# Optimization experiments

Hardware: AMD Instinct MI355X
Metric: run time of the kernel (lower is better)

The kernel has to match this reference:

```python
import jax, jax.numpy as jnp
import numpy as np

N_NODES = 4096
N_GRAPHS = 32
N = N_NODES * N_GRAPHS          # 131072 total nodes
DEG = 32
E = N * DEG                      # 4194304 edges
IN_CH = 16
OUT_CH = 2
EPS_BN = 1e-5


def setup_inputs() -> dict:
    key = jax.random.key(0)
    ks = jax.random.split(key, 24)
    rn = lambda k, s, scale=0.1: (jax.random.normal(k, s, dtype=jnp.float32) * scale)
    return {
        "x": jax.random.normal(ks[0], (N, IN_CH), dtype=jnp.float32),
        "edge_index": jax.random.randint(ks[1], (2, E), 0, N),
        "edge_attr": jax.random.uniform(ks[2], (E, 3), dtype=jnp.float32),
        # GraphConv1: 16 -> 20  (lin_rel has bias, lin_root has no bias; PyG GraphConv)
        "W_rel1": rn(ks[3], (IN_CH, 20)), "b1": jnp.zeros((20,), jnp.float32), "W_root1": rn(ks[4], (IN_CH, 20)),
        # GraphConv2: 20 -> 20
        "W_rel2": rn(ks[5], (20, 20)), "b2": jnp.zeros((20,), jnp.float32), "W_root2": rn(ks[6], (20, 20)),
        # GraphConv3: 20 -> 1
        "W_rel3": rn(ks[7], (20, 1)), "b3": jnp.zeros((1,), jnp.float32), "W_root3": rn(ks[8], (20, 1)),
        # BatchNorm1d(num_nodes) affine params (channel dim = node index)
        "bn1_g": jnp.ones((N_NODES,), jnp.float32), "bn1_b": jnp.zeros((N_NODES,), jnp.float32),
        "bn2_g": jnp.ones((N_NODES,), jnp.float32), "bn2_b": jnp.zeros((N_NODES,), jnp.float32),
        # fc layers, stored [in, out]
        "fc1_W": rn(ks[9], (N_NODES, 50), 0.02), "fc1_b": jnp.zeros((50,), jnp.float32),
        "fc2_W": rn(ks[10], (50, OUT_CH)), "fc2_b": jnp.zeros((OUT_CH,), jnp.float32),
        "num_graphs": N_GRAPHS,
    }


def _graph_conv(x, src, dst, w, W_rel, b_rel, W_root):
    # PyG GraphConv: out_i = lin_root(x_i) + lin_rel( sum_{j->i} w_ji * x_j )
    msg = x[src] * w[:, None]                              # [E, F] gather + scale
    agg = jax.ops.segment_sum(msg, dst, num_segments=x.shape[0])  # scatter-add
    return agg @ W_rel + b_rel + x @ W_root


def _bn_nodes(h3, gamma, beta):
    # BatchNorm1d(num_nodes) in training mode: h3 is [B, num_nodes, F];
    # normalize per node-channel over (batch, feat), biased variance (torch training).
    mu = jnp.mean(h3, axis=(0, 2), keepdims=True)
    var = jnp.var(h3, axis=(0, 2), keepdims=True)
    hn = (h3 - mu) * jax.lax.rsqrt(var + EPS_BN)
    return hn * gamma[None, :, None] + beta[None, :, None]


def reference(x, edge_index, edge_attr,
              W_rel1, b1, W_root1, W_rel2, b2, W_root2, W_rel3, b3, W_root3,
              bn1_g, bn1_b, bn2_g, bn2_b, fc1_W, fc1_b, fc2_W, fc2_b, num_graphs):
    src, dst = edge_index[0], edge_index[1]
    w = edge_attr[:, 2]
    B = num_graphs

    h = _graph_conv(x, src, dst, w, W_rel1, b1, W_root1)
    h = jax.nn.leaky_relu(h)                                   # slope 0.01, matches torch default
    h = _bn_nodes(h.reshape(B, -1, h.shape[-1]), bn1_g, bn1_b).reshape(-1, h.shape[-1])

    h = _graph_conv(h, src, dst, w, W_rel2, b2, W_root2)
    h = jax.nn.leaky_relu(h)
    h = _bn_nodes(h.reshape(B, -1, h.shape[-1]), bn2_g, bn2_b).reshape(-1, h.shape[-1])

    h = _graph_conv(h, src, dst, w, W_rel3, b3, W_root3)
    h = jax.nn.leaky_relu(h)
    h = h.reshape(B, -1)                                        # [B, num_nodes]

    # per-graph normalization; note: divides by var (not std), var is unbiased (torch.var default)
    eps = 1e-10
    out = (h - jnp.mean(h, axis=1, keepdims=True)) / (jnp.var(h, axis=1, keepdims=True, ddof=1) + eps)
    out = jax.nn.leaky_relu(out @ fc1_W + fc1_b)
    # dropout omitted (eval-mode identity)
    out = out @ fc2_W + fc2_b
    return (out, h)
```

## Files before the change

kernel.cpp:

```cpp
#include <hip/hip_runtime.h>
#include <hip/hip_fp16.h>

#define N_NODES 4096
#define N_GRAPHS 32
#define NTOT (N_NODES * N_GRAPHS)
#define NE (NTOT * 32)
#define C1 16
#define C2 20
#define CAP 72

#define NBUCK 512
#define BSHIFT 8
#define BMASK 255
#define CAPB 8960
#define EPB1 8192

__device__ __forceinline__ float lrelu(float v) { return v > 0.f ? v : 0.01f * v; }

__device__ __forceinline__ unsigned pack_edge(int src, float w) {
    int k = __float2int_rn(w * 32768.f);
    if (k > 32767) k = 32767;
    return (unsigned)src | ((unsigned)k << 17);
}
__device__ __forceinline__ void unpack_edge(unsigned p, int& src, float& w) {
    src = (int)(p & 0x1FFFFu);
    w = (float)(p >> 17) * 3.0517578125e-5f;
}

__device__ __forceinline__ uint4 pack8h(const float* v) {
    union { uint4 u4; __half h[8]; } c;
#pragma unroll
    for (int q = 0; q < 8; q++) c.h[q] = __float2half(v[q]);
    return c.u4;
}
__device__ __forceinline__ uint2 pack4h(const float* v) {
    union { uint2 u2; __half h[4]; } c;
#pragma unroll
    for (int q = 0; q < 4; q++) c.h[q] = __float2half(v[q]);
    return c.u2;
}
__device__ __forceinline__ void fma8(uint4 u, float wv, float* acc) {
    union { uint4 u4; __half2 h2[4]; } c; c.u4 = u;
#pragma unroll
    for (int q = 0; q < 4; q++) {
        float2 f = __half22float2(c.h2[q]);
        acc[2 * q]     += f.x * wv;
        acc[2 * q + 1] += f.y * wv;
    }
}
__device__ __forceinline__ void fma4(uint2 u, float wv, float* acc) {
    union { uint2 u2; __half2 h2[2]; } c; c.u2 = u;
#pragma unroll
    for (int q = 0; q < 2; q++) {
        float2 f = __half22float2(c.h2[q]);
        acc[2 * q]     += f.x * wv;
        acc[2 * q + 1] += f.y * wv;
    }
}
__device__ __forceinline__ void unp8(uint4 u, float* v) {
    union { uint4 u4; __half2 h2[4]; } c; c.u4 = u;
#pragma unroll
    for (int q = 0; q < 4; q++) {
        float2 f = __half22float2(c.h2[q]);
        v[2 * q] = f.x; v[2 * q + 1] = f.y;
    }
}
__device__ __forceinline__ void unp4(uint2 u, float* v) {
    union { uint2 u2; __half2 h2[2]; } c; c.u2 = u;
#pragma unroll
    for (int q = 0; q < 2; q++) {
        float2 f = __half22float2(c.h2[q]);
        v[2 * q] = f.x; v[2 * q + 1] = f.y;
    }
}

__global__ __launch_bounds__(256) void k_part1(const int* __restrict__ ei,
                                               const float* __restrict__ ea,
                                               int* __restrict__ gcur,
                                               uint2* __restrict__ part) {
    __shared__ unsigned lrecA[EPB1];
    __shared__ unsigned char lrecB[EPB1];
    __shared__ int hist[NBUCK], sscan[NBUCK], base[NBUCK], lcur[NBUCK];
    __shared__ int ts[256];
    int t = threadIdx.x;
    hist[t] = 0; hist[t + 256] = 0;
    __syncthreads();
    int eb = blockIdx.x * EPB1;
    int dreg[EPB1 / 256];
#pragma unroll
    for (int i = 0; i < EPB1 / 256; i++) {
        int d = ei[NE + eb + i * 256 + t];
        dreg[i] = d;
        atomicAdd(&hist[d >> BSHIFT], 1);
    }
    __syncthreads();
    int a0 = hist[2 * t], a1 = hist[2 * t + 1];
    ts[t] = a0 + a1;
    __syncthreads();
    for (int d = 1; d < 256; d <<= 1) {
        int v = (t >= d) ? ts[t - d] : 0;
        __syncthreads();
        ts[t] += v;
        __syncthreads();
    }
    int excl = (t == 0) ? 0 : ts[t - 1];
    sscan[2 * t] = excl;
    sscan[2 * t + 1] = excl + a0;
    lcur[2 * t] = excl;
    lcur[2 * t + 1] = excl + a0;
    base[t]       = atomicAdd(&gcur[t], hist[t]);
    base[t + 256] = atomicAdd(&gcur[t + 256], hist[t + 256]);
    __syncthreads();
#pragma unroll
    for (int i = 0; i < EPB1 / 256; i++) {
        int e = eb + i * 256 + t;
        int d = dreg[i];
        int b = d >> BSHIFT;
        int pos = atomicAdd(&lcur[b], 1);
        lrecA[pos] = pack_edge(ei[e], ea[3 * e + 2]);
        lrecB[pos] = (unsigned char)(d & BMASK);
    }
    __syncthreads();
    for (int j = t; j < EPB1; j += 256) {
        int lo = 0, hi = NBUCK - 1;
        while (lo < hi) { int mid = (lo + hi + 1) >> 1; if (sscan[mid] <= j) lo = mid; else hi = mid - 1; }
        int b = lo;
        int dp = base[b] + (j - sscan[b]);
        if (dp < CAPB) part[(size_t)b * CAPB + dp] = make_uint2(lrecA[j], (unsigned)lrecB[j]);
    }
}

__global__ __launch_bounds__(256) void k_part2(const int* __restrict__ gcur,
                                               const uint2* __restrict__ part,
                                               unsigned* __restrict__ slots,
                                               int* __restrict__ cnt) {
    __shared__ int cur[256];
    int t = threadIdx.x;
    cur[t] = 0;
    __syncthreads();
    int b = blockIdx.x;
    int nrec = gcur[b]; if (nrec > CAPB) nrec = CAPB;
    const uint2* rp = part + (size_t)b * CAPB;
    int nb = b << BSHIFT;
    for (int i = t; i < nrec; i += 256) {
        uint2 r = rp[i];
        int ld = (int)r.y;
        int pos = atomicAdd(&cur[ld], 1);
        if (pos < CAP) slots[(size_t)pos * NTOT + nb + ld] = r.x;
    }
    __syncthreads();
    cnt[nb + t] = cur[t];
}

__global__ void k_fill_slots(const int* __restrict__ ei, const float* __restrict__ ea,
                             int* __restrict__ cnt, unsigned* __restrict__ slots) {
    int e = blockIdx.x * 256 + threadIdx.x;
    if (e >= NE) return;
    int d = ei[NE + e];
    int pos = atomicAdd(&cnt[d], 1);
    if (pos < CAP) slots[(size_t)pos * NTOT + d] = pack_edge(ei[e], ea[3 * e + 2]);
}

__global__ void k_xcast(const float* __restrict__ x, uint4* __restrict__ xa, uint4* __restrict__ xb) {
    int n = blockIdx.x * 256 + threadIdx.x;
    if (n >= NTOT) return;
    float xr[C1];
    const float4* xp = (const float4*)(x + (size_t)n * C1);
#pragma unroll
    for (int q = 0; q < 4; q++) ((float4*)xr)[q] = xp[q];
    xa[n] = pack8h(xr);
    xb[n] = pack8h(xr + 8);
}

__global__ __launch_bounds__(256) void k_conv1(const uint4* __restrict__ xa, const uint4* __restrict__ xb,
                        const unsigned* __restrict__ slots, const int* __restrict__ cnt,
                        const float* __restrict__ Wr, const float* __restrict__ bb,
                        const float* __restrict__ Wo, float* __restrict__ t1) {
    __shared__ float sWr[C1 * C2], sWo[C1 * C2], sb[C2];
    __shared__ float sacc[4][64][8];
    for (int k = threadIdx.x; k < C1 * C2; k += 256) { sWr[k] = Wr[k]; sWo[k] = Wo[k]; }
    if (threadIdx.x < C2) sb[threadIdx.x] = bb[threadIdx.x];
    int nl = threadIdx.x & 63;
    int sub = threadIdx.x >> 6;
    int gn = blockIdx.x * 64 + nl;
    int m = cnt[gn]; if (m > CAP) m = CAP;
    int h0 = m >> 1;
    int lo = (sub & 1) ? h0 : 0;
    int hi = (sub & 1) ? m : h0;
    const uint4* va = (sub < 2) ? xa : xb;
    float acc[8];
#pragma unroll
    for (int q = 0; q < 8; q++) acc[q] = 0.f;
    int i = lo;
    for (; i + 4 <= hi; i += 4) {
        unsigned p0 = __builtin_nontemporal_load(slots + (size_t)(i + 0) * NTOT + gn);
        unsigned p1 = __builtin_nontemporal_load(slots + (size_t)(i + 1) * NTOT + gn);
        unsigned p2 = __builtin_nontemporal_load(slots + (size_t)(i + 2) * NTOT + gn);
        unsigned p3 = __builtin_nontemporal_load(slots + (size_t)(i + 3) * NTOT + gn);
        int s0, s1, s2, s3; float w0, w1, w2, w3;
        unpack_edge(p0, s0, w0); unpack_edge(p1, s1, w1);
        unpack_edge(p2, s2, w2); unpack_edge(p3, s3, w3);
        uint4 u0 = va[s0], u1 = va[s1], u2 = va[s2], u3 = va[s3];
        fma8(u0, w0, acc); fma8(u1, w1, acc); fma8(u2, w2, acc); fma8(u3, w3, acc);
    }
    for (; i < hi; i++) {
        unsigned p = __builtin_nontemporal_load(slots + (size_t)i * NTOT + gn);
        int s; float w; unpack_edge(p, s, w);
        fma8(va[s], w, acc);
    }
#pragma unroll
    for (int q = 0; q < 8; q++) sacc[sub][nl][q] = acc[q];
    __syncthreads();
    int n2 = threadIdx.x >> 2, qq = threadIdx.x & 3;
    int gn2 = blockIdx.x * 64 + n2;
    float accf[C1];
#pragma unroll
    for (int q = 0; q < 8; q++) accf[q] = sacc[0][n2][q] + sacc[1][n2][q];
#pragma unroll
    for (int q = 0; q < 8; q++) accf[8 + q] = sacc[2][n2][q] + sacc[3][n2][q];
    float xr[C1];
    unp8(xa[gn2], xr); unp8(xb[gn2], xr + 8);
    float outv[5];
#pragma unroll
    for (int jj = 0; jj < 5; jj++) {
        int j = qq * 5 + jj;
        float a = sb[j];
#pragma unroll
        for (int q = 0; q < C1; q++) a += accf[q] * sWr[q * C2 + j] + xr[q] * sWo[q * C2 + j];
        outv[jj] = lrelu(a);
    }
#pragma unroll
    for (int jj = 0; jj < 5; jj++) t1[(size_t)gn2 * C2 + qq * 5 + jj] = outv[jj];
}

__global__ void k_stats(const float* __restrict__ t, float* __restrict__ mu, float* __restrict__ rs) {
    int i = blockIdx.x;
    float s = 0.f, ss = 0.f;
    for (int k = threadIdx.x; k < N_GRAPHS * C2; k += 64) {
        int g = k / C2, j = k - g * C2;
        float v = t[((size_t)(g * N_NODES + i)) * C2 + j];
        s += v; ss += v * v;
    }
#pragma unroll
    for (int off = 32; off > 0; off >>= 1) { s += __shfl_down(s, off); ss += __shfl_down(ss, off); }
    if (threadIdx.x == 0) {
        float m = s * (1.f / (N_GRAPHS * C2));
        float var = ss * (1.f / (N_GRAPHS * C2)) - m * m;
        mu[i] = m;
        rs[i] = rsqrtf(var + 1e-5f);
    }
}

__global__ void k_bn_apply(const float* __restrict__ t, const float* __restrict__ mu,
                           const float* __restrict__ rs, const float* __restrict__ gam,
                           const float* __restrict__ bet, uint4* __restrict__ hnA,
                           uint2* __restrict__ hnB) {
    int n = blockIdx.x * 256 + threadIdx.x;
    if (n >= NTOT) return;
    int i = n & (N_NODES - 1);
    float sc = rs[i] * gam[i];
    float sh = bet[i] - mu[i] * sc;
    float v[C2];
    const float4* tp = (const float4*)(t + (size_t)n * C2);
#pragma unroll
    for (int q = 0; q < 5; q++) ((float4*)v)[q] = tp[q];
#pragma unroll
    for (int j = 0; j < C2; j++) v[j] = v[j] * sc + sh;
    hnA[n] = pack8h(v);
    uint2* hp = hnB + (size_t)n * 3;
    hp[0] = pack4h(v + 8);
    hp[1] = pack4h(v + 12);
    hp[2] = pack4h(v + 16);
}

__global__ __launch_bounds__(256) void k_conv2(const uint4* __restrict__ hnA,
                        const uint2* __restrict__ hnB,
                        const unsigned* __restrict__ slots, const int* __restrict__ cnt,
                        const float* __restrict__ Wr, const float* __restrict__ bb,
                        const float* __restrict__ Wo, float* __restrict__ t2) {
    __shared__ float sWr[C2 * C2], sWo[C2 * C2], sb[C2];
    __shared__ float saccA[2][64][8];
    __shared__ float saccB[2][64][12];
    for (int k = threadIdx.x; k < C2 * C2; k += 256) { sWr[k] = Wr[k]; sWo[k] = Wo[k]; }
    if (threadIdx.x < C2) sb[threadIdx.x] = bb[threadIdx.x];
    int nl = threadIdx.x & 63;
    int sub = threadIdx.x >> 6;
    int gn = blockIdx.x * 64 + nl;
    int m = cnt[gn]; if (m > CAP) m = CAP;
    int h0 = m >> 1;
    int lo = (sub & 1) ? h0 : 0;
    int hi = (sub & 1) ? m : h0;
    if (sub < 2) {
        float acc[8];
#pragma unroll
        for (int q = 0; q < 8; q++) acc[q] = 0.f;
        int i = lo;
        for (; i + 4 <= hi; i += 4) {
            unsigned p0 = __builtin_nontemporal_load(slots + (size_t)(i + 0) * NTOT + gn);
            unsigned p1 = __builtin_nontemporal_load(slots + (size_t)(i + 1) * NTOT + gn);
            unsigned p2 = __builtin_nontemporal_load(slots + (size_t)(i + 2) * NTOT + gn);
            unsigned p3 = __builtin_nontemporal_load(slots + (size_t)(i + 3) * NTOT + gn);
            int s0, s1, s2, s3; float w0, w1, w2, w3;
            unpack_edge(p0, s0, w0); unpack_edge(p1, s1, w1);
            unpack_edge(p2, s2, w2); unpack_edge(p3, s3, w3);
            uint4 u0 = hnA[s0], u1 = hnA[s1], u2 = hnA[s2], u3 = hnA[s3];
            fma8(u0, w0, acc); fma8(u1, w1, acc); fma8(u2, w2, acc); fma8(u3, w3, acc);
        }
        for (; i < hi; i++) {
            unsigned p = __builtin_nontemporal_load(slots + (size_t)i * NTOT + gn);
            int s; float w; unpack_edge(p, s, w);
            fma8(hnA[s], w, acc);
        }
#pragma unroll
        for (int q = 0; q < 8; q++) saccA[sub][nl][q] = acc[q];
    } else {
        float acc[12];
#pragma unroll
        for (int q = 0; q < 12; q++) acc[q] = 0.f;
        int i = lo;
        for (; i + 4 <= hi; i += 4) {
            unsigned p0 = __builtin_nontemporal_load(slots + (size_t)(i + 0) * NTOT + gn);
            unsigned p1 = __builtin_nontemporal_load(slots + (size_t)(i + 1) * NTOT + gn);
            unsigned p2 = __builtin_nontemporal_load(slots + (size_t)(i + 2) * NTOT + gn);
            unsigned p3 = __builtin_nontemporal_load(slots + (size_t)(i + 3) * NTOT + gn);
            int s0, s1, s2, s3; float w0, w1, w2, w3;
            unpack_edge(p0, s0, w0); unpack_edge(p1, s1, w1);
            unpack_edge(p2, s2, w2); unpack_edge(p3, s3, w3);
            const uint2* r0 = hnB + (size_t)s0 * 3;
            const uint2* r1 = hnB + (size_t)s1 * 3;
            const uint2* r2 = hnB + (size_t)s2 * 3;
            const uint2* r3 = hnB + (size_t)s3 * 3;
            uint2 a0 = r0[0], b0 = r0[1], c0 = r0[2];
            uint2 a1 = r1[0], b1 = r1[1], c1 = r1[2];
            uint2 a2 = r2[0], b2 = r2[1], c2 = r2[2];
            uint2 a3 = r3[0], b3 = r3[1], c3 = r3[2];
            fma4(a0, w0, acc); fma4(b0, w0, acc + 4); fma4(c0, w0, acc + 8);
            fma4(a1, w1, acc); fma4(b1, w1, acc + 4); fma4(c1, w1, acc + 8);
            fma4(a2, w2, acc); fma4(b2, w2, acc + 4); fma4(c2, w2, acc + 8);
            fma4(a3, w3, acc); fma4(b3, w3, acc + 4); fma4(c3, w3, acc + 8);
        }
        for (; i < hi; i++) {
            unsigned p = __builtin_nontemporal_load(slots + (size_t)i * NTOT + gn);
            int s; float w; unpack_edge(p, s, w);
            const uint2* r = hnB + (size_t)s * 3;
            fma4(r[0], w, acc); fma4(r[1], w, acc + 4); fma4(r[2], w, acc + 8);
        }
#pragma unroll
        for (int q = 0; q < 12; q++) saccB[sub - 2][nl][q] = acc[q];
    }
    __syncthreads();
    int n2 = threadIdx.x >> 2, qq = threadIdx.x & 3;
    int gn2 = blockIdx.x * 64 + n2;
    float accf[C2];
#pragma unroll
    for (int q = 0; q < 8; q++) accf[q] = saccA[0][n2][q] + saccA[1][n2][q];
#pragma unroll
    for (int q = 0; q < 12; q++) accf[8 + q] = saccB[0][n2][q] + saccB[1][n2][q];
    float h[C2];
    unp8(hnA[gn2], h);
    {
        const uint2* r = hnB + (size_t)gn2 * 3;
        unp4(r[0], h + 8); unp4(r[1], h + 12); unp4(r[2], h + 16);
    }
    float outv[5];
#pragma unroll
    for (int jj = 0; jj < 5; jj++) {
        int j = qq * 5 + jj;
        float a = sb[j];
#pragma unroll
        for (int q = 0; q < C2; q++) a += accf[q] * sWr[q * C2 + j] + h[q] * sWo[q * C2 + j];
        outv[jj] = lrelu(a);
    }
#pragma unroll
    for (int jj = 0; jj < 5; jj++) t2[(size_t)gn2 * C2 + qq * 5 + jj] = outv[jj];
}

__global__ void k_bn2_proj(const float* __restrict__ t, const float* __restrict__ mu,
                           const float* __restrict__ rs, const float* __restrict__ gam,
                           const float* __restrict__ bet, const float* __restrict__ Wr3,
                           const float* __restrict__ b3, const float* __restrict__ Wo3,
                           float* __restrict__ y, float* __restrict__ r2) {
    __shared__ float sWr[C2], sWo[C2];
    if (threadIdx.x < C2) { sWr[threadIdx.x] = Wr3[threadIdx.x]; sWo[threadIdx.x] = Wo3[threadIdx.x]; }
    __syncthreads();
    int n = blockIdx.x * 256 + threadIdx.x;
    if (n >= NTOT) return;
    int i = n & (N_NODES - 1);
    float sc = rs[i] * gam[i];
    float sh = bet[i] - mu[i] * sc;
    float v[C2];
    const float4* tp = (const float4*)(t + (size_t)n * C2);
#pragma unroll
    for (int q = 0; q < 5; q++) ((float4*)v)[q] = tp[q];
    float ay = 0.f, ar = 0.f;
#pragma unroll
    for (int j = 0; j < C2; j++) {
        float hv = v[j] * sc + sh;
        ay += hv * sWr[j];
        ar += hv * sWo[j];
    }
    y[n] = ay;
    r2[n] = ar + b3[0];
}

__global__ __launch_bounds__(256) void k_conv3(const float* __restrict__ y, const float* __restrict__ r2,
                        const unsigned* __restrict__ slots, const int* __restrict__ cnt,
                        float* __restrict__ hout, float* __restrict__ gsum, float* __restrict__ gss) {
    __shared__ float pbuf[2][128];
    __shared__ float ls[4], lss[4];
    int nl = threadIdx.x & 127;
    int half = threadIdx.x >> 7;
    int n = blockIdx.x * 128 + nl;
    int m = cnt[n]; if (m > CAP) m = CAP;
    int h0 = m >> 1;
    int lo = half ? h0 : 0;
    int hi = half ? m : h0;
    float a = 0.f;
    int i = lo;
    for (; i + 4 <= hi; i += 4) {
        unsigned p0 = __builtin_nontemporal_load(slots + (size_t)(i + 0) * NTOT + n);
        unsigned p1 = __builtin_nontemporal_load(slots + (size_t)(i + 1) * NTOT + n);
        unsigned p2 = __builtin_nontemporal_load(slots + (size_t)(i + 2) * NTOT + n);
        unsigned p3 = __builtin_nontemporal_load(slots + (size_t)(i + 3) * NTOT + n);
        int s0, s1, s2, s3; float w0, w1, w2, w3;
        unpack_edge(p0, s0, w0); unpack_edge(p1, s1, w1);
        unpack_edge(p2, s2, w2); unpack_edge(p3, s3, w3);
        a += y[s0] * w0 + y[s1] * w1 + y[s2] * w2 + y[s3] * w3;
    }
    for (; i < hi; i++) {
        unsigned p = __builtin_nontemporal_load(slots + (size_t)i * NTOT + n);
        int s; float w; unpack_edge(p, s, w);
        a += y[s] * w;
    }
    pbuf[half][nl] = a;
    __syncthreads();
    float v = 0.f;
    if (half == 0) {
        v = lrelu(pbuf[0][nl] + pbuf[1][nl] + r2[n]);
        hout[n] = v;
    }
    float s = v, ss = v * v;
#pragma unroll
    for (int o = 32; o > 0; o >>= 1) { s += __shfl_down(s, o); ss += __shfl_down(ss, o); }
    int wid = threadIdx.x >> 6, lid = threadIdx.x & 63;
    if (lid == 0) { ls[wid] = s; lss[wid] = ss; }
    __syncthreads();
    if (threadIdx.x == 0) {
        int g = blockIdx.x >> 5;
        atomicAdd(&gsum[g], ls[0] + ls[1] + ls[2] + ls[3]);
        atomicAdd(&gss[g], lss[0] + lss[1] + lss[2] + lss[3]);
    }
}

__global__ void k_fc1(const float* __restrict__ h, const float* __restrict__ gsum,
                      const float* __restrict__ gss, const float* __restrict__ W,
                      const float* __restrict__ b, float* __restrict__ z) {
    __shared__ float ls[4];
    int blk = blockIdx.x;
    int g = blk / 50, k = blk - g * 50;
    float mu = gsum[g] / N_NODES;
    float var = (gss[g] - N_NODES * mu * mu) / (N_NODES - 1);
    float inv = 1.f / (var + 1e-10f);
    const float* hr = h + (size_t)g * N_NODES;
    float p = 0.f;
    for (int n = threadIdx.x; n < N_NODES; n += 256)
        p += (hr[n] - mu) * inv * W[(size_t)n * 50 + k];
#pragma unroll
    for (int off = 32; off > 0; off >>= 1) p += __shfl_down(p, off);
    int wid = threadIdx.x >> 6, lid = threadIdx.x & 63;
    if (lid == 0) ls[wid] = p;
    __syncthreads();
    if (threadIdx.x == 0) {
        float S = ls[0] + ls[1] + ls[2] + ls[3];
        z[g * 50 + k] = lrelu(S + b[k]);
    }
}

__global__ void k_fc2(const float* __restrict__ z, const float* __restrict__ W,
                      const float* __restrict__ b, float* __restrict__ out) {
    int t = threadIdx.x;
    if (t >= N_GRAPHS * 2) return;
    int g = t >> 1, o = t & 1;
    float acc = b[o];
#pragma unroll
    for (int k = 0; k < 50; k++) acc += z[g * 50 + k] * W[k * 2 + o];
    out[g * 2 + o] = acc;
}

extern "C" void kernel_launch(void* const* d_in, const int* in_sizes, int n_in,
                              void* d_out, int out_size, void* d_ws, size_t ws_size,
                              hipStream_t stream) {
    const float* x    = (const float*)d_in[0];
    const int*   ei   = (const int*)d_in[1];
    const float* ea   = (const float*)d_in[2];
    const float* Wr1  = (const float*)d_in[3];
    const float* b1   = (const float*)d_in[4];
    const float* Wo1  = (const float*)d_in[5];
    const float* Wr2  = (const float*)d_in[6];
    const float* b2   = (const float*)d_in[7];
    const float* Wo2  = (const float*)d_in[8];
    const float* Wr3  = (const float*)d_in[9];
    const float* b3   = (const float*)d_in[10];
    const float* Wo3  = (const float*)d_in[11];
    const float* bn1g = (const float*)d_in[12];
    const float* bn1b = (const float*)d_in[13];
    const float* bn2g = (const float*)d_in[14];
    const float* bn2b = (const float*)d_in[15];
    const float* fc1W = (const float*)d_in[16];
    const float* fc1b = (const float*)d_in[17];
    const float* fc2W = (const float*)d_in[18];
    const float* fc2b = (const float*)d_in[19];
    float* out = (float*)d_out;

    const size_t part_bytes  = (size_t)NBUCK * CAPB * sizeof(uint2);
    const size_t slots_bytes = (size_t)NTOT * CAP * sizeof(unsigned);
    const size_t tail_bytes  = (size_t)NTOT * C2 * sizeof(float)
                             + (size_t)NTOT * 16 * 3
                             + (size_t)NTOT * 24
                             + (size_t)NTOT * 2 * sizeof(float)
                             + (size_t)NTOT * sizeof(int)
                             + (size_t)(NBUCK + 4 * N_NODES + 8 * N_GRAPHS + N_GRAPHS * 50 + 64) * sizeof(float);
    const bool useSort = ws_size >= part_bytes + slots_bytes + tail_bytes;

    char* wsb = (char*)d_ws;
    uint2*    part  = (uint2*)wsb;     wsb += useSort ? part_bytes : 0;
    unsigned* slots = (unsigned*)wsb;  wsb += slots_bytes;
    float*    bufA  = (float*)wsb;     wsb += (size_t)NTOT * C2 * sizeof(float);
    uint4*    xa    = (uint4*)wsb;     wsb += (size_t)NTOT * 16;
    uint4*    xb    = (uint4*)wsb;     wsb += (size_t)NTOT * 16;
    uint4*    hnA   = (uint4*)wsb;     wsb += (size_t)NTOT * 16;
    uint2*    hnB   = (uint2*)wsb;     wsb += (size_t)NTOT * 24;
    float*    yv    = (float*)wsb;     wsb += (size_t)NTOT * sizeof(float);
    float*    r2v   = (float*)wsb;     wsb += (size_t)NTOT * sizeof(float);
    int*      cnt   = (int*)wsb;       wsb += (size_t)NTOT * sizeof(int);
    int*      gcur  = (int*)wsb;       wsb += NBUCK * sizeof(int);
    float*    mu1   = (float*)wsb;     wsb += N_NODES * sizeof(float);
    float*    rs1   = (float*)wsb;     wsb += N_NODES * sizeof(float);
    float*    mu2   = (float*)wsb;     wsb += N_NODES * sizeof(float);
    float*    rs2   = (float*)wsb;     wsb += N_NODES * sizeof(float);
    float*    gsum  = (float*)wsb;     wsb += N_GRAPHS * sizeof(float);
    float*    gss   = (float*)wsb;     wsb += N_GRAPHS * sizeof(float);
    float*    z     = (float*)wsb;     wsb += N_GRAPHS * 50 * sizeof(float);

    const int EB = (NE + 255) / 256;
    const int NB = (NTOT + 255) / 256;

    hipMemsetAsync(gsum, 0, 2 * N_GRAPHS * sizeof(float), stream);
    k_xcast<<<NB, 256, 0, stream>>>(x, xa, xb);
    if (useSort) {
        hipMemsetAsync(gcur, 0, NBUCK * sizeof(int), stream);
        k_part1<<<NE / EPB1, 256, 0, stream>>>(ei, ea, gcur, part);
        k_part2<<<NBUCK, 256, 0, stream>>>(gcur, part, slots, cnt);
    } else {
        hipMemsetAsync(cnt, 0, (size_t)NTOT * sizeof(int), stream);
        k_fill_slots<<<EB, 256, 0, stream>>>(ei, ea, cnt, slots);
    }

    k_conv1<<<NTOT / 64, 256, 0, stream>>>(xa, xb, slots, cnt, Wr1, b1, Wo1, bufA);
    k_stats<<<N_NODES, 64, 0, stream>>>(bufA, mu1, rs1);
    k_bn_apply<<<NB, 256, 0, stream>>>(bufA, mu1, rs1, bn1g, bn1b, hnA, hnB);

    k_conv2<<<NTOT / 64, 256, 0, stream>>>(hnA, hnB, slots, cnt, Wr2, b2, Wo2, bufA);
    k_stats<<<N_NODES, 64, 0, stream>>>(bufA, mu2, rs2);
    k_bn2_proj<<<NB, 256, 0, stream>>>(bufA, mu2, rs2, bn2g, bn2b, Wr3, b3, Wo3, yv, r2v);

    k_conv3<<<NTOT / 128, 256, 0, stream>>>(yv, r2v, slots, cnt, out + 64, gsum, gss);

    k_fc1<<<N_GRAPHS * 50, 256, 0, stream>>>(out + 64, gsum, gss, fc1W, fc1b, z);
    k_fc2<<<1, 64, 0, stream>>>(z, fc2W, fc2b, out);
}
```

Measured before the change: 488.9 us.

## Stage slot scatter in LDS and restructure conv gathers with deeper unrolling

k_part2 now splits each bucket across two blocks and builds the per-destination slot tile in shared memory, then writes it out row-coalesced instead of scattering 4-byte stores directly to global. The conv1/conv2 kernels switch to 128 nodes per block with two threads per node, each gathering all feature chunks over half the edges, using 8-way unrolled gather helpers. The conv2 feature layout is changed from three 8-byte pieces per node to one 16-byte plus one 8-byte array, cutting the number of load instructions. The edge-slot loads are now read once per feature chunk, which adds repeated slot traffic, and the shared tile uses about 37 KB of LDS per block, limiting occupancy.

Measured after the change: 512.7 us. +4.9%, slower.

```diff
diff --git a/kernel.cpp b/kernel.cpp
--- a/kernel.cpp
+++ b/kernel.cpp
@@ -71,6 +71,47 @@
     for (int q = 0; q < 2; q++) {
         float2 f = __half22float2(c.h2[q]);
         v[2 * q] = f.x; v[2 * q + 1] = f.y;
+    }
+}
+
+__device__ __forceinline__ void gather16(const uint4* __restrict__ arr,
+                                         const unsigned* __restrict__ slots,
+                                         int gn, int lo, int hi, float* acc) {
+    int i = lo;
+    for (; i + 8 <= hi; i += 8) {
+        unsigned p[8];
+#pragma unroll
+        for (int k = 0; k < 8; k++) p[k] = __builtin_nontemporal_load(slots + (size_t)(i + k) * NTOT + gn);
+        uint4 u[8]; float w[8];
+#pragma unroll
+        for (int k = 0; k < 8; k++) { int s; unpack_edge(p[k], s, w[k]); u[k] = arr[s]; }
+#pragma unroll
+        for (int k = 0; k < 8; k++) fma8(u[k], w[k], acc);
+    }
+    for (; i < hi; i++) {
+        unsigned p = __builtin_nontemporal_load(slots + (size_t)i * NTOT + gn);
+        int s; float w; unpack_edge(p, s, w);
+        fma8(arr[s], w, acc);
+    }
+}
+__device__ __forceinline__ void gather8(const uint2* __restrict__ arr,
+                                        const unsigned* __restrict__ slots,
+                                        int gn, int lo, int hi, float* acc) {
+    int i = lo;
+    for (; i + 8 <= hi; i += 8) {
+        unsigned p[8];
+#pragma unroll
+        for (int k = 0; k < 8; k++) p[k] = __builtin_nontemporal_load(slots + (size_t)(i + k) * NTOT + gn);
+        uint2 u[8]; float w[8];
+#pragma unroll
+        for (int k = 0; k < 8; k++) { int s; unpack_edge(p[k], s, w[k]); u[k] = arr[s]; }
+#pragma unroll
+        for (int k = 0; k < 8; k++) fma4(u[k], w[k], acc);
+    }
+    for (; i < hi; i++) {
+        unsigned p = __builtin_nontemporal_load(slots + (size_t)i * NTOT + gn);
+        int s; float w; unpack_edge(p, s, w);
+        fma4(arr[s], w, acc);
     }
 }
 
@@ -134,22 +175,35 @@
                                                const uint2* __restrict__ part,
                                                unsigned* __restrict__ slots,
                                                int* __restrict__ cnt) {
-    __shared__ int cur[256];
+    __shared__ unsigned tile[128 * CAP];
+    __shared__ int cur[128];
+    __shared__ int maxc;
     int t = threadIdx.x;
-    cur[t] = 0;
-    __syncthreads();
-    int b = blockIdx.x;
+    if (t < 128) cur[t] = 0;
+    if (t == 0) maxc = 0;
+    __syncthreads();
+    int b = blockIdx.x >> 1;
+    int halfsel = blockIdx.x & 1;
+    int nbase = (b << BSHIFT) + (halfsel << 7);
     int nrec = gcur[b]; if (nrec > CAPB) nrec = CAPB;
     const uint2* rp = part + (size_t)b * CAPB;
-    int nb = b << BSHIFT;
     for (int i = t; i < nrec; i += 256) {
         uint2 r = rp[i];
         int ld = (int)r.y;
-        int pos = atomicAdd(&cur[ld], 1);
-        if (pos < CAP) slots[(size_t)pos * NTOT + nb + ld] = r.x;
-    }
-    __syncthreads();
-    cnt[nb + t] = cur[t];
+        if ((ld >> 7) == halfsel) {
+            int l = ld & 127;
+            int pos = atomicAdd(&cur[l], 1);
+            if (pos < CAP) tile[pos * 128 + l] = r.x;
+        }
+    }
+    __syncthreads();
+    if (t < 128) { cnt[nbase + t] = cur[t]; atomicMax(&maxc, cur[t]); }
+    __syncthreads();
+    int mc = maxc; if (mc > CAP) mc = CAP;
+    for (int j = t; j < mc * 128; j += 256) {
+        int pos = j >> 7, l = j & 127;
+        slots[(size_t)pos * NTOT + nbase + l] = tile[j];
+    }
 }
 
 __global__ void k_fill_slots(const int* __restrict__ ei, const float* __restrict__ ea,
@@ -177,60 +231,42 @@
                         const float* __restrict__ Wr, const float* __restrict__ bb,
                         const float* __restrict__ Wo, float* __restrict__ t1) {
     __shared__ float sWr[C1 * C2], sWo[C1 * C2], sb[C2];
-    __shared__ float sacc[4][64][8];
+    __shared__ float sacc[2][128][17];
     for (int k = threadIdx.x; k < C1 * C2; k += 256) { sWr[k] = Wr[k]; sWo[k] = Wo[k]; }
     if (threadIdx.x < C2) sb[threadIdx.x] = bb[threadIdx.x];
-    int nl = threadIdx.x & 63;
-    int sub = threadIdx.x >> 6;
-    int gn = blockIdx.x * 64 + nl;
+    int nl = threadIdx.x & 127;
+    int half = threadIdx.x >> 7;
+    int gn = blockIdx.x * 128 + nl;
     int m = cnt[gn]; if (m > CAP) m = CAP;
     int h0 = m >> 1;
-    int lo = (sub & 1) ? h0 : 0;
-    int hi = (sub & 1) ? m : h0;
-    const uint4* va = (sub < 2) ? xa : xb;
-    float acc[8];
-#pragma unroll
-    for (int q = 0; q < 8; q++) acc[q] = 0.f;
-    int i = lo;
-    for (; i + 4 <= hi; i += 4) {
-        unsigned p0 = __builtin_nontemporal_load(slots + (size_t)(i + 0) * NTOT + gn);
-        unsigned p1 = __builtin_nontemporal_load(slots + (size_t)(i + 1) * NTOT + gn);
-        unsigned p2 = __builtin_nontemporal_load(slots + (size_t)(i + 2) * NTOT + gn);
-        unsigned p3 = __builtin_nontemporal_load(slots + (size_t)(i + 3) * NTOT + gn);
-        int s0, s1, s2, s3; float w0, w1, w2, w3;
-        unpack_edge(p0, s0, w0); unpack_edge(p1, s1, w1);
-        unpack_edge(p2, s2, w2); unpack_edge(p3, s3, w3);
-        uint4 u0 = va[s0], u1 = va[s1], u2 = va[s2], u3 = va[s3];
-        fma8(u0, w0, acc); fma8(u1, w1, acc); fma8(u2, w2, acc); fma8(u3, w3, acc);
-    }
-    for (; i < hi; i++) {
-        unsigned p = __builtin_nontemporal_load(slots + (size_t)i * NTOT + gn);
-        int s; float w; unpack_edge(p, s, w);
-        fma8(va[s], w, acc);
-    }
-#pragma unroll
-    for (int q = 0; q < 8; q++) sacc[sub][nl][q] = acc[q];
-    __syncthreads();
-    int n2 = threadIdx.x >> 2, qq = threadIdx.x & 3;
-    int gn2 = blockIdx.x * 64 + n2;
+    int lo = half ? h0 : 0;
+    int hi = half ? m : h0;
+    float acc[C1];
+#pragma unroll
+    for (int q = 0; q < C1; q++) acc[q] = 0.f;
+    gather16(xa, slots, gn, lo, hi, acc);
+    gather16(xb, slots, gn, lo, hi, acc + 8);
+#pragma unroll
+    for (int q = 0; q < C1; q++) sacc[half][nl][q] = acc[q];
+    __syncthreads();
+    int n2 = threadIdx.x >> 1, oh = threadIdx.x & 1;
+    int gn2 = blockIdx.x * 128 + n2;
     float accf[C1];
 #pragma unroll
-    for (int q = 0; q < 8; q++) accf[q] = sacc[0][n2][q] + sacc[1][n2][q];
-#pragma unroll
-    for (int q = 0; q < 8; q++) accf[8 + q] = sacc[2][n2][q] + sacc[3][n2][q];
+    for (int q = 0; q < C1; q++) accf[q] = sacc[0][n2][q] + sacc[1][n2][q];
     float xr[C1];
     unp8(xa[gn2], xr); unp8(xb[gn2], xr + 8);
-    float outv[5];
-#pragma unroll
-    for (int jj = 0; jj < 5; jj++) {
-        int j = qq * 5 + jj;
+    float outv[10];
+#pragma unroll
+    for (int jj = 0; jj < 10; jj++) {
+        int j = oh * 10 + jj;
         float a = sb[j];
 #pragma unroll
         for (int q = 0; q < C1; q++) a += accf[q] * sWr[q * C2 + j] + xr[q] * sWo[q * C2 + j];
         outv[jj] = lrelu(a);
     }
 #pragma unroll
-    for (int jj = 0; jj < 5; jj++) t1[(size_t)gn2 * C2 + qq * 5 + jj] = outv[jj];
+    for (int jj = 0; jj < 10; jj++) t1[(size_t)gn2 * C2 + oh * 10 + jj] = outv[jj];
 }
 
 __global__ void k_stats(const float* __restrict__ t, float* __restrict__ mu, float* __restrict__ rs) {
@@ -254,7 +290,7 @@
 __global__ void k_bn_apply(const float* __restrict__ t, const float* __restrict__ mu,
                            const float* __restrict__ rs, const float* __restrict__ gam,
                            const float* __restrict__ bet, uint4* __restrict__ hnA,
-                           uint2* __restrict__ hnB) {
+                           uint4* __restrict__ hnB1, uint2* __restrict__ hnB2) {
     int n = blockIdx.x * 256 + threadIdx.x;
     if (n >= NTOT) return;
     int i = n & (N_NODES - 1);
@@ -267,112 +303,53 @@
 #pragma unroll
     for (int j = 0; j < C2; j++) v[j] = v[j] * sc + sh;
     hnA[n] = pack8h(v);
-    uint2* hp = hnB + (size_t)n * 3;
-    hp[0] = pack4h(v + 8);
-    hp[1] = pack4h(v + 12);
-    hp[2] = pack4h(v + 16);
+    hnB1[n] = pack8h(v + 8);
+    hnB2[n] = pack4h(v + 16);
 }
 
 __global__ __launch_bounds__(256) void k_conv2(const uint4* __restrict__ hnA,
-                        const uint2* __restrict__ hnB,
+                        const uint4* __restrict__ hnB1, const uint2* __restrict__ hnB2,
                         const unsigned* __restrict__ slots, const int* __restrict__ cnt,
                         const float* __restrict__ Wr, const float* __restrict__ bb,
                         const float* __restrict__ Wo, float* __restrict__ t2) {
     __shared__ float sWr[C2 * C2], sWo[C2 * C2], sb[C2];
-    __shared__ float saccA[2][64][8];
-    __shared__ float saccB[2][64][12];
+    __shared__ float sacc[2][128][21];
     for (int k = threadIdx.x; k < C2 * C2; k += 256) { sWr[k] = Wr[k]; sWo[k] = Wo[k]; }
     if (threadIdx.x < C2) sb[threadIdx.x] = bb[threadIdx.x];
-    int nl = threadIdx.x & 63;
-    int sub = threadIdx.x >> 6;
-    int gn = blockIdx.x * 64 + nl;
+    int nl = threadIdx.x & 127;
+    int half = threadIdx.x >> 7;
+    int gn = blockIdx.x * 128 + nl;
     int m = cnt[gn]; if (m > CAP) m = CAP;
     int h0 = m >> 1;
-    int lo = (sub & 1) ? h0 : 0;
-    int hi = (sub & 1) ? m : h0;
-    if (sub < 2) {
-        float acc[8];
-#pragma unroll
-        for (int q = 0; q < 8; q++) acc[q] = 0.f;
-        int i = lo;
-        for (; i + 4 <= hi; i += 4) {
-            unsigned p0 = __builtin_nontemporal_load(slots + (size_t)(i + 0) * NTOT + gn);
-            unsigned p1 = __builtin_nontemporal_load(slots + (size_t)(i + 1) * NTOT + gn);
-            unsigned p2 = __builtin_nontemporal_load(slots + (size_t)(i + 2) * NTOT + gn);
-            unsigned p3 = __builtin_nontemporal_load(slots + (size_t)(i + 3) * NTOT + gn);
-            int s0, s1, s2, s3; float w0, w1, w2, w3;
-            unpack_edge(p0, s0, w0); unpack_edge(p1, s1, w1);
-            unpack_edge(p2, s2, w2); unpack_edge(p3, s3, w3);
-            uint4 u0 = hnA[s0], u1 = hnA[s1], u2 = hnA[s2], u3 = hnA[s3];
-            fma8(u0, w0, acc); fma8(u1, w1, acc); fma8(u2, w2, acc); fma8(u3, w3, acc);
-        }
-        for (; i < hi; i++) {
-            unsigned p = __builtin_nontemporal_load(slots + (size_t)i * NTOT + gn);
-            int s; float w; unpack_edge(p, s, w);
-            fma8(hnA[s], w, acc);
-        }
-#pragma unroll
-        for (int q = 0; q < 8; q++) saccA[sub][nl][q] = acc[q];
-    } else {
-        float acc[12];
-#pragma unroll
-        for (int q = 0; q < 12; q++) acc[q] = 0.f;
-        int i = lo;
-        for (; i + 4 <= hi; i += 4) {
-            unsigned p0 = __builtin_nontemporal_load(slots + (size_t)(i + 0) * NTOT + gn);
-            unsigned p1 = __builtin_nontemporal_load(slots + (size_t)(i + 1) * NTOT + gn);
-            unsigned p2 = __builtin_nontemporal_load(slots + (size_t)(i + 2) * NTOT + gn);
-            unsigned p3 = __builtin_nontemporal_load(slots + (size_t)(i + 3) * NTOT + gn);
-            int s0, s1, s2, s3; float w0, w1, w2, w3;
-            unpack_edge(p0, s0, w0); unpack_edge(p1, s1, w1);
-            unpack_edge(p2, s2, w2); unpack_edge(p3, s3, w3);
-            const uint2* r0 = hnB + (size_t)s0 * 3;
-            const uint2* r1 = hnB + (size_t)s1 * 3;
-            const uint2* r2 = hnB + (size_t)s2 * 3;
-            const uint2* r3 = hnB + (size_t)s3 * 3;
-            uint2 a0 = r0[0], b0 = r0[1], c0 = r0[2];
-            uint2 a1 = r1[0], b1 = r1[1], c1 = r1[2];
-            uint2 a2 = r2[0], b2 = r2[1], c2 = r2[2];
-            uint2 a3 = r3[0], b3 = r3[1], c3 = r3[2];
-            fma4(a0, w0, acc); fma4(b0, w0, acc + 4); fma4(c0, w0, acc + 8);
-            fma4(a1, w1, acc); fma4(b1, w1, acc + 4); fma4(c1, w1, acc + 8);
-            fma4(a2, w2, acc); fma4(b2, w2, acc + 4); fma4(c2, w2, acc + 8);
-            fma4(a3, w3, acc); fma4(b3, w3, acc + 4); fma4(c3, w3, acc + 8);
-        }
-        for (; i < hi; i++) {
-            unsigned p = __builtin_nontemporal_load(slots + (size_t)i * NTOT + gn);
-            int s; float w; unpack_edge(p, s, w);
-            const uint2* r = hnB + (size_t)s * 3;
-            fma4(r[0], w, acc); fma4(r[1], w, acc + 4); fma4(r[2], w, acc + 8);
-        }
-#pragma unroll
-        for (int q = 0; q < 12; q++) saccB[sub - 2][nl][q] = acc[q];
-    }
-    __syncthreads();
-    int n2 = threadIdx.x >> 2, qq = threadIdx.x & 3;
-    int gn2 = blockIdx.x * 64 + n2;
+    int lo = half ? h0 : 0;
+    int hi = half ? m : h0;
+    float acc[C2];
+#pragma unroll
+    for (int q = 0; q < C2; q++) acc[q] = 0.f;
+    gather16(hnA, slots, gn, lo, hi, acc);
+    gather16(hnB1, slots, gn, lo, hi, acc + 8);
+    gather8(hnB2, slots, gn, lo, hi, acc + 16);
+#pragma unroll
+    for (int q = 0; q < C2; q++) sacc[half][nl][q] = acc[q];
+    __syncthreads();
+    int n2 = threadIdx.x >> 1, oh = threadIdx.x & 1;
+    int gn2 = blockIdx.x * 128 + n2;
     float accf[C2];
 #pragma unroll
-    for (int q = 0; q < 8; q++) accf[q] = saccA[0][n2][q] + saccA[1][n2][q];
-#pragma unroll
-    for (int q = 0; q < 12; q++) accf[8 + q] = saccB[0][n2][q] + saccB[1][n2][q];
+    for (int q = 0; q < C2; q++) accf[q] = sacc[0][n2][q] + sacc[1][n2][q];
     float h[C2];
-    unp8(hnA[gn2], h);
-    {
-        const uint2* r = hnB + (size_t)gn2 * 3;
-        unp4(r[0], h + 8); unp4(r[1], h + 12); unp4(r[2], h + 16);
-    }
-    float outv[5];
-#pragma unroll
-    for (int jj = 0; jj < 5; jj++) {
-        int j = qq * 5 + jj;
+    unp8(hnA[gn2], h); unp8(hnB1[gn2], h + 8); unp4(hnB2[gn2], h + 16);
+    float outv[10];
+#pragma unroll
+    for (int jj = 0; jj < 10; jj++) {
+        int j = oh * 10 + jj;
         float a = sb[j];
 #pragma unroll
         for (int q = 0; q < C2; q++) a += accf[q] * sWr[q * C2 + j] + h[q] * sWo[q * C2 + j];
         outv[jj] = lrelu(a);
     }
 #pragma unroll
-    for (int jj = 0; jj < 5; jj++) t2[(size_t)gn2 * C2 + qq * 5 + jj] = outv[jj];
+    for (int jj = 0; jj < 10; jj++) t2[(size_t)gn2 * C2 + oh * 10 + jj] = outv[jj];
 }
 
 __global__ void k_bn2_proj(const float* __restrict__ t, const float* __restrict__ mu,
@@ -417,15 +394,12 @@
     int hi = half ? m : h0;
     float a = 0.f;
     int i = lo;
-    for (; i + 4 <= hi; i += 4) {
-        unsigned p0 = __builtin_nontemporal_load(slots + (size_t)(i + 0) * NTOT + n);
-        unsigned p1 = __builtin_nontemporal_load(slots + (size_t)(i + 1) * NTOT + n);
-        unsigned p2 = __builtin_nontemporal_load(slots + (size_t)(i + 2) * NTOT + n);
-        unsigned p3 = __builtin_nontemporal_load(slots + (size_t)(i + 3) * NTOT + n);
-        int s0, s1, s2, s3; float w0, w1, w2, w3;
-        unpack_edge(p0, s0, w0); unpack_edge(p1, s1, w1);
-        unpack_edge(p2, s2, w2); unpack_edge(p3, s3, w3);
-        a += y[s0] * w0 + y[s1] * w1 + y[s2] * w2 + y[s3] * w3;
+    for (; i + 8 <= hi; i += 8) {
+        unsigned p[8];
+#pragma unroll
+        for (int k = 0; k < 8; k++) p[k] = __builtin_nontemporal_load(slots + (size_t)(i + k) * NTOT + n);
+#pragma unroll
+        for (int k = 0; k < 8; k++) { int s; float w; unpack_edge(p[k], s, w); a += y[s] * w; }
     }
     for (; i < hi; i++) {
         unsigned p = __builtin_nontemporal_load(slots + (size_t)i * NTOT + n);
@@ -515,8 +489,8 @@
     const size_t part_bytes  = (size_t)NBUCK * CAPB * sizeof(uint2);
     const size_t slots_bytes = (size_t)NTOT * CAP * sizeof(unsigned);
     const size_t tail_bytes  = (size_t)NTOT * C2 * sizeof(float)
-                             + (size_t)NTOT * 16 * 3
-                             + (size_t)NTOT * 24
+                             + (size_t)NTOT * 16 * 4
+                             + (size_t)NTOT * 8
                              + (size_t)NTOT * 2 * sizeof(float)
                              + (size_t)NTOT * sizeof(int)
                              + (size_t)(NBUCK + 4 * N_NODES + 8 * N_GRAPHS + N_GRAPHS * 50 + 64) * sizeof(float);
@@ -529,7 +503,8 @@
     uint4*    xa    = (uint4*)wsb;     wsb += (size_t)NTOT * 16;
     uint4*    xb    = (uint4*)wsb;     wsb += (size_t)NTOT * 16;
     uint4*    hnA   = (uint4*)wsb;     wsb += (size_t)NTOT * 16;
-    uint2*    hnB   = (uint2*)wsb;     wsb += (size_t)NTOT * 24;
+    uint4*    hnB1  = (uint4*)wsb;     wsb += (size_t)NTOT * 16;
+    uint2*    hnB2  = (uint2*)wsb;     wsb += (size_t)NTOT * 8;
     float*    yv    = (float*)wsb;     wsb += (size_t)NTOT * sizeof(float);
     float*    r2v   = (float*)wsb;     wsb += (size_t)NTOT * sizeof(float);
     int*      cnt   = (int*)wsb;       wsb += (size_t)NTOT * sizeof(int);
@@ -550,17 +525,17 @@
     if (useSort) {
         hipMemsetAsync(gcur, 0, NBUCK * sizeof(int), stream);
         k_part1<<<NE / EPB1, 256, 0, stream>>>(ei, ea, gcur, part);
-        k_part2<<<NBUCK, 256, 0, stream>>>(gcur, part, slots, cnt);
+        k_part2<<<NBUCK * 2, 256, 0, stream>>>(gcur, part, slots, cnt);
     } else {
         hipMemsetAsync(cnt, 0, (size_t)NTOT * sizeof(int), stream);
         k_fill_slots<<<EB, 256, 0, stream>>>(ei, ea, cnt, slots);
     }
 
-    k_conv1<<<NTOT / 64, 256, 0, stream>>>(xa, xb, slots, cnt, Wr1, b1, Wo1, bufA);
+    k_conv1<<<NTOT / 128, 256, 0, stream>>>(xa, xb, slots, cnt, Wr1, b1, Wo1, bufA);
     k_stats<<<N_NODES, 64, 0, stream>>>(bufA, mu1, rs1);
-    k_bn_apply<<<NB, 256, 0, stream>>>(bufA, mu1, rs1, bn1g, bn1b, hnA, hnB);
-
-    k_conv2<<<NTOT / 64, 256, 0, stream>>>(hnA, hnB, slots, cnt, Wr2, b2, Wo2, bufA);
+    k_bn_apply<<<NB, 256, 0, stream>>>(bufA, mu1, rs1, bn1g, bn1b, hnA, hnB1, hnB2);
+
+    k_conv2<<<NTOT / 128, 256, 0, stream>>>(hnA, hnB1, hnB2, slots, cnt, Wr2, b2, Wo2, bufA);
     k_stats<<<N_NODES, 64, 0, stream>>>(bufA, mu2, rs2);
     k_bn2_proj<<<NB, 256, 0, stream>>>(bufA, mu2, rs2, bn2g, bn2b, Wr3, b3, Wo3, yv, r2v);
 
```
